# Kernel optimization log

Measured on AMD Instinct MI355X. Metric: run time of the kernel, lower is better.

The kernel has to match this reference:

```python
import jax, jax.numpy as jnp
import numpy as np

IMAGE_W = 640
IMAGE_H = 640
MIN_SCORE = 0.05
NMS_THR = 0.5
MAX_DET = 100
B, A, C = 8, 76725, 80  # batch, total anchors over FPN levels (640x640, 9 anchors/loc), COCO classes


def setup_inputs() -> dict:
    key = jax.random.key(0)
    k1, k2, k3, k4, k5, k6 = jax.random.split(key, 6)
    # sigmoid-like class scores in [0,1]
    cls_heads = jax.random.uniform(k1, (B, A, C), dtype=jnp.float32)
    reg_heads = jax.random.normal(k2, (B, A, 4), dtype=jnp.float32) * 0.5
    # plausible anchors: centers in image, sizes in [16,256]
    cx = jax.random.uniform(k3, (B, A), dtype=jnp.float32) * IMAGE_W
    cy = jax.random.uniform(k4, (B, A), dtype=jnp.float32) * IMAGE_H
    w = jax.random.uniform(k5, (B, A), dtype=jnp.float32, minval=16.0, maxval=256.0)
    h = jax.random.uniform(k6, (B, A), dtype=jnp.float32, minval=16.0, maxval=256.0)
    batch_anchors = jnp.stack([cx - 0.5 * w, cy - 0.5 * h, cx + 0.5 * w, cy + 0.5 * h], axis=-1)
    return {"cls_heads": cls_heads, "reg_heads": reg_heads, "batch_anchors": batch_anchors}


def _decode(reg, anchors):
    # snap_tx_ty_tw_th_to_x1_y1_x2_y2: [A,4] deltas + [A,4] anchors -> int boxes
    wh = anchors[:, 2:] - anchors[:, :2]
    ctr = anchors[:, :2] + 0.5 * wh
    reg = reg * jnp.array([0.1, 0.1, 0.2, 0.2], dtype=reg.dtype)
    pwh = jnp.exp(reg[:, 2:]) * wh
    pctr = reg[:, :2] * wh + ctr
    boxes = jnp.concatenate([pctr - 0.5 * pwh, pctr + 0.5 * pwh], axis=1)
    boxes = boxes.astype(jnp.int32)  # torch .int() truncates toward zero, same as astype
    x1 = jnp.maximum(boxes[:, 0], 0)
    y1 = jnp.maximum(boxes[:, 1], 0)
    x2 = jnp.minimum(boxes[:, 2], IMAGE_W - 1)
    y2 = jnp.minimum(boxes[:, 3], IMAGE_H - 1)
    return jnp.stack([x1, y1, x2, y2], axis=1)


def _single_image(cls, reg, anchors):
    boxes = _decode(reg, anchors)              # [A,4] int32
    bf = boxes.astype(jnp.float32)
    scores = jnp.max(cls, axis=1)              # [A]
    classes = jnp.argmax(cls, axis=1)          # [A] int
    areas = (bf[:, 2] - bf[:, 0]) * (bf[:, 3] - bf[:, 1])
    work = jnp.where(scores > MIN_SCORE, scores, -jnp.inf)
    out_s = jnp.full((MAX_DET,), -1.0, jnp.float32)
    out_c = jnp.full((MAX_DET,), -1.0, jnp.float32)
    out_b = jnp.full((MAX_DET, 4), -1.0, jnp.float32)

    # Greedy global pick + per-class suppression == per-class NMS followed by
    # global descending sort + top MAX_DET (classes are independent under NMS).
    def body(i, carry):
        work, out_s, out_c, out_b = carry
        idx = jnp.argmax(work)
        s = work[idx]
        ok = jnp.isfinite(s)
        box = bf[idx]
        cls_i = classes[idx]
        xx1 = jnp.maximum(bf[:, 0], box[0])
        yy1 = jnp.maximum(bf[:, 1], box[1])
        xx2 = jnp.minimum(bf[:, 2], box[2])
        yy2 = jnp.minimum(bf[:, 3], box[3])
        inter = jnp.maximum(xx2 - xx1, 0.0) * jnp.maximum(yy2 - yy1, 0.0)
        union = areas + areas[idx] - inter
        iou = jnp.where(union > 0, inter / jnp.where(union > 0, union, 1.0), 0.0)
        suppress = (classes == cls_i) & (iou >= NMS_THR)  # keep mask was iou < thr
        work = jnp.where(ok & suppress, -jnp.inf, work)
        work = work.at[idx].set(-jnp.inf)
        out_s = out_s.at[i].set(jnp.where(ok, s, -1.0))
        out_c = out_c.at[i].set(jnp.where(ok, cls_i.astype(jnp.float32), -1.0))
        out_b = out_b.at[i].set(jnp.where(ok, box, -1.0))
        return (work, out_s, out_c, out_b)

    _, out_s, out_c, out_b = jax.lax.fori_loop(0, MAX_DET, body, (work, out_s, out_c, out_b))
    return out_s, out_c, out_b


def reference(cls_heads, reg_heads, batch_anchors):
    return jax.vmap(_single_image)(cls_heads, reg_heads, batch_anchors)
```

## Files before the change

### kernel.cpp

```cpp
#include <hip/hip_runtime.h>

#define NB 8
#define NA 76725
#define NC 80
#define MAXDET 100
#define CAP  1024
#define FTHR 0x3F7FF994u
#define TILE 64
#define NBLK 1199
#define ST4  21

__device__ inline unsigned long long shfl_down_u64(unsigned long long v, int o) {
    unsigned lo = (unsigned)v, hi = (unsigned)(v >> 32);
    lo = __shfl_down(lo, o);
    hi = __shfl_down(hi, o);
    return ((unsigned long long)hi << 32) | lo;
}

__device__ inline unsigned long long shfl_xor_u64(unsigned long long v, int m) {
    unsigned lo = __shfl_xor((unsigned)v, m), hi = __shfl_xor((unsigned)(v >> 32), m);
    return ((unsigned long long)hi << 32) | lo;
}

__device__ inline bool iou_ge_half(float ax1, float ay1, float ax2, float ay2, float aar,
                                   float bx1, float by1, float bx2, float by2, float bar) {
    float xx1 = fmaxf(ax1, bx1), yy1 = fmaxf(ay1, by1);
    float xx2 = fminf(ax2, bx2), yy2 = fminf(ay2, by2);
    float inter = fmaxf(xx2 - xx1, 0.0f) * fmaxf(yy2 - yy1, 0.0f);
    float un = aar + bar - inter;
    float iou = (un > 0.0f) ? inter / un : 0.0f;
    return iou >= 0.5f;
}

__global__ __launch_bounds__(256) void k_map(const float* __restrict__ cls,
                                             const float* __restrict__ reg,
                                             const float* __restrict__ anc,
                                             unsigned long long* __restrict__ keys,
                                             unsigned long long* __restrict__ boxes,
                                             ulonglong2* __restrict__ cand,
                                             unsigned int* __restrict__ cnt_p,
                                             unsigned int* __restrict__ vws) {
    __shared__ float4 sc[TILE * ST4];
    __shared__ unsigned s_v[4];
    const int b = blockIdx.y;
    const int n0 = blockIdx.x * TILE;
    const int ait = min(TILE, NA - n0);
    const int tid = threadIdx.x;
    const size_t base4 = ((size_t)b * NA + n0) * (NC / 4);
    const int nq = ait * (NC / 4);

#pragma unroll
    for (int k = 0; k < 5; ++k) {
        int q = tid + k * 256;
        if (q < nq) {
            float4 v = reinterpret_cast<const float4*>(cls)[base4 + q];
            sc[(q / 20) * ST4 + (q % 20)] = v;
        }
    }
    __syncthreads();

    const int a = tid >> 2, t = tid & 3;
    float best = -1.0f; int bc = 0;
#pragma unroll
    for (int j = 0; j < 5; ++j) {
        float4 v = sc[a * ST4 + t * 5 + j];
        if (v.x > best) { best = v.x; bc = t * 20 + 4 * j + 0; }
        if (v.y > best) { best = v.y; bc = t * 20 + 4 * j + 1; }
        if (v.z > best) { best = v.z; bc = t * 20 + 4 * j + 2; }
        if (v.w > best) { best = v.w; bc = t * 20 + 4 * j + 3; }
    }
    unsigned long long pk = ((unsigned long long)__float_as_uint(best) << 8)
                          | (unsigned)(255 - bc);
    pk = max(pk, shfl_xor_u64(pk, 1));
    pk = max(pk, shfl_xor_u64(pk, 2));

    bool valid = false, sel = false;
    unsigned long long key = 0ull, bp = 0ull;
    if (t == 0 && a < ait) {
        unsigned sbits = (unsigned)(pk >> 8);
        int cg = 255 - (int)(pk & 0xFFull);
        const int n_img = n0 + a;
        const size_t n = (size_t)b * NA + n_img;
        float4 rg = reinterpret_cast<const float4*>(reg)[n];
        float4 an = reinterpret_cast<const float4*>(anc)[n];

        float wx = __fsub_rn(an.z, an.x);
        float wy = __fsub_rn(an.w, an.y);
        float cx = __fadd_rn(an.x, __fmul_rn(0.5f, wx));
        float cy = __fadd_rn(an.y, __fmul_rn(0.5f, wy));
        float tx = __fmul_rn(rg.x, 0.1f), ty = __fmul_rn(rg.y, 0.1f);
        float tw = __fmul_rn(rg.z, 0.2f), th = __fmul_rn(rg.w, 0.2f);
        float pw = __fmul_rn(expf(tw), wx);
        float ph = __fmul_rn(expf(th), wy);
        float px = __fadd_rn(__fmul_rn(tx, wx), cx);
        float py = __fadd_rn(__fmul_rn(ty, wy), cy);
        int x1 = (int)__fsub_rn(px, __fmul_rn(0.5f, pw));
        int y1 = (int)__fsub_rn(py, __fmul_rn(0.5f, ph));
        int x2 = (int)__fadd_rn(px, __fmul_rn(0.5f, pw));
        int y2 = (int)__fadd_rn(py, __fmul_rn(0.5f, ph));
        x1 = max(x1, 0); y1 = max(y1, 0); x2 = min(x2, 639); y2 = min(y2, 639);

        bp = (unsigned long long)(unsigned short)(short)x1
           | ((unsigned long long)(unsigned short)(short)y1 << 16)
           | ((unsigned long long)(unsigned short)(short)x2 << 32)
           | ((unsigned long long)(unsigned short)(short)y2 << 48);
        float bestf = __uint_as_float(sbits);
        if (bestf > 0.05f) {
            unsigned inv = 0x1FFFFu - (unsigned)n_img;
            key = ((unsigned long long)sbits << 32) | ((unsigned long long)inv << 7)
                | (unsigned)cg;
            valid = true;
            sel = sbits >= FTHR;
        }
        keys[n] = key;
        boxes[n] = bp;
    }

    const int lane = tid & 63;
    const int wid = tid >> 6;

    unsigned long long bal = __ballot(valid);
    if (lane == 0) s_v[wid] = (unsigned)__popcll(bal);

    unsigned long long sbal = __ballot(sel);
    unsigned base = 0;
    if (lane == 0 && sbal) base = atomicAdd(&cnt_p[b * 32], (unsigned)__popcll(sbal));
    base = __shfl(base, 0);
    if (sel) {
        unsigned off = base + (unsigned)__popcll(sbal & ((1ull << lane) - 1ull));
        if (off < CAP) {
            ulonglong2 e; e.x = key; e.y = bp;
            cand[(size_t)b * CAP + off] = e;
        }
    }

    __syncthreads();
    if (tid == 0)
        vws[(size_t)b * NBLK + blockIdx.x] = s_v[0] + s_v[1] + s_v[2] + s_v[3];
}

__global__ __launch_bounds__(512) void k_nms(const ulonglong2* __restrict__ cand,
                                             const unsigned int* __restrict__ cnt_p,
                                             const unsigned int* __restrict__ vws,
                                             unsigned int* __restrict__ flag,
                                             float* __restrict__ out) {
    __shared__ unsigned long long sk[CAP];
    __shared__ unsigned long long sb[CAP];
    __shared__ int s_np;
    __shared__ unsigned s_ws[8];
    __shared__ unsigned s_vsum;
    const int b = blockIdx.x;
    unsigned total = cnt_p[b * 32];
    bool overflow = total > CAP;
    unsigned m = overflow ? CAP : total;

    unsigned local = 0;
    for (int j = threadIdx.x; j < NBLK; j += 512) local += vws[(size_t)b * NBLK + j];
    for (int o = 32; o > 0; o >>= 1) local += __shfl_down(local, o);
    if ((threadIdx.x & 63) == 0) s_ws[threadIdx.x >> 6] = local;

    for (int i = threadIdx.x; i < CAP; i += 512) {
        if (i < (int)m) { ulonglong2 e = cand[(size_t)b * CAP + i]; sk[i] = e.x; sb[i] = e.y; }
        else            { sk[i] = 0ull; sb[i] = 0ull; }
    }
    __syncthreads();
    if (threadIdx.x == 0) {
        unsigned s = 0;
        for (int w = 0; w < 8; ++w) s += s_ws[w];
        s_vsum = s;
    }

    for (int k = 2; k <= CAP; k <<= 1) {
        for (int j = k >> 1; j > 0; j >>= 1) {
            __syncthreads();
            int t = threadIdx.x;
            int i = ((t & ~(j - 1)) << 1) | (t & (j - 1));
            int l = i | j;
            unsigned long long ki = sk[i], kl = sk[l];
            bool desc = (i & k) == 0;
            if (desc ? (ki < kl) : (ki > kl)) {
                sk[i] = kl; sk[l] = ki;
                unsigned long long tmp = sb[i]; sb[i] = sb[l]; sb[l] = tmp;
            }
        }
    }
    __syncthreads();

    if (threadIdx.x < 64) {
        const int lane = threadIdx.x;
        float q0x1 = 0, q0y1 = 0, q0x2 = 0, q0y2 = 0, q0a = 0; int q0c = -1;
        float q1x1 = 0, q1y1 = 0, q1x2 = 0, q1y2 = 0, q1a = 0; int q1c = -1;
        int np = 0;
        unsigned long long nk = (m > 0) ? sk[0] : 0ull;
        unsigned long long nbx = (m > 0) ? sb[0] : 0ull;
        for (int jj = 0; jj < (int)m && np < MAXDET; ++jj) {
            unsigned long long key = nk;
            unsigned long long bx = nbx;
            if (jj + 1 < (int)m) { nk = sk[jj + 1]; nbx = sb[jj + 1]; }
            if (!key) break;
            int ci = (int)(key & 0x7Full);
            float x1 = (float)(short)(bx & 0xFFFF);
            float y1 = (float)(short)((bx >> 16) & 0xFFFF);
            float x2 = (float)(short)((bx >> 32) & 0xFFFF);
            float y2 = (float)(short)((bx >> 48) & 0xFFFF);
            float ar = (x2 - x1) * (y2 - y1);
            bool sup = false;
            if (lane < np && q0c == ci)
                sup = iou_ge_half(q0x1, q0y1, q0x2, q0y2, q0a, x1, y1, x2, y2, ar);
            if (64 + lane < np && q1c == ci)
                sup = sup || iou_ge_half(q1x1, q1y1, q1x2, q1y2, q1a, x1, y1, x2, y2, ar);
            if (__ballot(sup) != 0ull) continue;
            int s = np;
            if (s < 64) {
                if (lane == s) {
                    q0x1 = x1; q0y1 = y1; q0x2 = x2; q0y2 = y2; q0a = ar; q0c = ci;
                    out[b * MAXDET + s] = __uint_as_float((unsigned)(key >> 32));
                    out[NB * MAXDET + b * MAXDET + s] = (float)ci;
                    float* ob = out + 2 * NB * MAXDET + (size_t)(b * MAXDET + s) * 4;
                    ob[0] = x1; ob[1] = y1; ob[2] = x2; ob[3] = y2;
                }
            } else {
                if (lane == s - 64) {
                    q1x1 = x1; q1y1 = y1; q1x2 = x2; q1y2 = y2; q1a = ar; q1c = ci;
                    out[b * MAXDET + s] = __uint_as_float((unsigned)(key >> 32));
                    out[NB * MAXDET + b * MAXDET + s] = (float)ci;
                    float* ob = out + 2 * NB * MAXDET + (size_t)(b * MAXDET + s) * 4;
                    ob[0] = x1; ob[1] = y1; ob[2] = x2; ob[3] = y2;
                }
            }
            ++np;
        }
        if (lane == 0) s_np = np;
    }
    __syncthreads();
    int np = s_np;
    bool fb = overflow || (np < MAXDET && s_vsum > m);
    if (threadIdx.x == 0) flag[b] = fb ? 1u : 0u;
    if (!fb) {
        for (int i = np + (int)threadIdx.x; i < MAXDET; i += 512) {
            out[b * MAXDET + i] = -1.0f;
            out[NB * MAXDET + b * MAXDET + i] = -1.0f;
            float* ob = out + 2 * NB * MAXDET + (size_t)(b * MAXDET + i) * 4;
            ob[0] = -1.0f; ob[1] = -1.0f; ob[2] = -1.0f; ob[3] = -1.0f;
        }
    }
}

__global__ __launch_bounds__(1024) void k_fallback(unsigned long long* __restrict__ keys,
                                                   const unsigned long long* __restrict__ boxes,
                                                   const unsigned int* __restrict__ flag,
                                                   float* __restrict__ out) {
    const int b = blockIdx.x;
    if (!flag[b]) return;
    __shared__ unsigned long long wm[16];
    __shared__ unsigned long long gbest;
    unsigned long long* kb = keys + (size_t)b * NA;
    const unsigned long long* bb = boxes + (size_t)b * NA;

    for (int it = 0; it < MAXDET; ++it) {
        unsigned long long best = 0ull;
        for (int i = threadIdx.x; i < NA; i += 1024) {
            unsigned long long k = kb[i];
            if (k > best) best = k;
        }
        for (int o = 32; o > 0; o >>= 1) {
            unsigned long long v = shfl_down_u64(best, o);
            if (v > best) best = v;
        }
        if ((threadIdx.x & 63) == 0) wm[threadIdx.x >> 6] = best;
        __syncthreads();
        if (threadIdx.x == 0) {
            unsigned long long g = wm[0];
            for (int w = 1; w < 16; ++w) if (wm[w] > g) g = wm[w];
            gbest = g;
        }
        __syncthreads();
        best = gbest;
        if (best == 0ull) {
            for (int s = it + (int)threadIdx.x; s < MAXDET; s += 1024) {
                out[b * MAXDET + s] = -1.0f;
                out[NB * MAXDET + b * MAXDET + s] = -1.0f;
                float* ob = out + 2 * NB * MAXDET + (size_t)(b * MAXDET + s) * 4;
                ob[0] = -1.0f; ob[1] = -1.0f; ob[2] = -1.0f; ob[3] = -1.0f;
            }
            break;
        }
        int ci = (int)(best & 0x7Full);
        int a = 0x1FFFF - (int)((best >> 7) & 0x1FFFFull);
        unsigned long long bx = bb[a];
        float x1 = (float)(short)(bx & 0xFFFF);
        float y1 = (float)(short)((bx >> 16) & 0xFFFF);
        float x2 = (float)(short)((bx >> 32) & 0xFFFF);
        float y2 = (float)(short)((bx >> 48) & 0xFFFF);
        float ar = (x2 - x1) * (y2 - y1);
        if (threadIdx.x == 0) {
            out[b * MAXDET + it] = __uint_as_float((unsigned)(best >> 32));
            out[NB * MAXDET + b * MAXDET + it] = (float)ci;
            float* ob = out + 2 * NB * MAXDET + (size_t)(b * MAXDET + it) * 4;
            ob[0] = x1; ob[1] = y1; ob[2] = x2; ob[3] = y2;
        }
        for (int i = threadIdx.x; i < NA; i += 1024) {
            unsigned long long kk = kb[i];
            if (!kk) continue;
            if (kk == best) { kb[i] = 0ull; continue; }
            if ((int)(kk & 0x7Full) != ci) continue;
            unsigned long long ob2 = bb[i];
            float u1 = (float)(short)(ob2 & 0xFFFF);
            float v1 = (float)(short)((ob2 >> 16) & 0xFFFF);
            float u2 = (float)(short)((ob2 >> 32) & 0xFFFF);
            float v2 = (float)(short)((ob2 >> 48) & 0xFFFF);
            float oar = (u2 - u1) * (v2 - v1);
            if (iou_ge_half(x1, y1, x2, y2, ar, u1, v1, u2, v2, oar)) kb[i] = 0ull;
        }
        __syncthreads();
    }
}

extern "C" void kernel_launch(void* const* d_in, const int* in_sizes, int n_in,
                              void* d_out, int out_size, void* d_ws, size_t ws_size,
                              hipStream_t stream) {
    const float* cls = (const float*)d_in[0];
    const float* reg = (const float*)d_in[1];
    const float* anc = (const float*)d_in[2];
    float* out = (float*)d_out;

    const size_t SZ_KEYS = (size_t)NB * NA * 8;
    unsigned long long* keys  = (unsigned long long*)d_ws;
    unsigned long long* boxes = (unsigned long long*)((char*)d_ws + SZ_KEYS);
    ulonglong2* cand = (ulonglong2*)((char*)d_ws + 2 * SZ_KEYS);
    unsigned* cnt_p = (unsigned*)((char*)d_ws + 2 * SZ_KEYS + (size_t)NB * CAP * 16);
    unsigned* vws   = cnt_p + NB * 32;
    unsigned* flag  = vws + (size_t)NB * NBLK;

    hipMemsetAsync(cnt_p, 0, NB * 32 * 4, stream);

    dim3 gmap(NBLK, NB);
    k_map<<<gmap, 256, 0, stream>>>(cls, reg, anc, keys, boxes, cand, cnt_p, vws);
    k_nms<<<NB, 512, 0, stream>>>(cand, cnt_p, vws, flag, out);
    k_fallback<<<NB, 1024, 0, stream>>>(keys, boxes, flag, out);
}
```

Before: 333.8 us.

## Make k_map persistent with register-prefetched next tile loads

Replaces the one-block-per-tile grid with a persistent grid of 192 blocks per image. Each block loops over tiles and prefetches the next tile's class scores, regression and anchor data into registers while it computes the current tile. Reg and anchor data are staged through shared memory, and the per-block valid counts shrink to 192 entries per image, which k_nms reads. This aims to hide global load latency in a memory-bound pass, at the cost of more registers per thread and lower occupancy.

Measured after the change: 333.0 us. Within noise of the previous version (-0.2%).

```diff
diff --git a/kernel.cpp b/kernel.cpp
--- a/kernel.cpp
+++ b/kernel.cpp
@@ -8,6 +8,7 @@
 #define FTHR 0x3F7FF994u
 #define TILE 64
 #define NBLK 1199
+#define GX   192
 #define ST4  21
 
 __device__ inline unsigned long long shfl_down_u64(unsigned long long v, int o) {
@@ -41,102 +42,131 @@
                                              unsigned int* __restrict__ cnt_p,
                                              unsigned int* __restrict__ vws) {
     __shared__ float4 sc[TILE * ST4];
+    __shared__ float4 s_rg[TILE];
+    __shared__ float4 s_an[TILE];
     __shared__ unsigned s_v[4];
     const int b = blockIdx.y;
-    const int n0 = blockIdx.x * TILE;
-    const int ait = min(TILE, NA - n0);
     const int tid = threadIdx.x;
-    const size_t base4 = ((size_t)b * NA + n0) * (NC / 4);
-    const int nq = ait * (NC / 4);
-
-#pragma unroll
-    for (int k = 0; k < 5; ++k) {
-        int q = tid + k * 256;
-        if (q < nq) {
-            float4 v = reinterpret_cast<const float4*>(cls)[base4 + q];
-            sc[(q / 20) * ST4 + (q % 20)] = v;
-        }
-    }
-    __syncthreads();
-
-    const int a = tid >> 2, t = tid & 3;
-    float best = -1.0f; int bc = 0;
-#pragma unroll
-    for (int j = 0; j < 5; ++j) {
-        float4 v = sc[a * ST4 + t * 5 + j];
-        if (v.x > best) { best = v.x; bc = t * 20 + 4 * j + 0; }
-        if (v.y > best) { best = v.y; bc = t * 20 + 4 * j + 1; }
-        if (v.z > best) { best = v.z; bc = t * 20 + 4 * j + 2; }
-        if (v.w > best) { best = v.w; bc = t * 20 + 4 * j + 3; }
-    }
-    unsigned long long pk = ((unsigned long long)__float_as_uint(best) << 8)
-                          | (unsigned)(255 - bc);
-    pk = max(pk, shfl_xor_u64(pk, 1));
-    pk = max(pk, shfl_xor_u64(pk, 2));
-
-    bool valid = false, sel = false;
-    unsigned long long key = 0ull, bp = 0ull;
-    if (t == 0 && a < ait) {
-        unsigned sbits = (unsigned)(pk >> 8);
-        int cg = 255 - (int)(pk & 0xFFull);
-        const int n_img = n0 + a;
-        const size_t n = (size_t)b * NA + n_img;
-        float4 rg = reinterpret_cast<const float4*>(reg)[n];
-        float4 an = reinterpret_cast<const float4*>(anc)[n];
-
-        float wx = __fsub_rn(an.z, an.x);
-        float wy = __fsub_rn(an.w, an.y);
-        float cx = __fadd_rn(an.x, __fmul_rn(0.5f, wx));
-        float cy = __fadd_rn(an.y, __fmul_rn(0.5f, wy));
-        float tx = __fmul_rn(rg.x, 0.1f), ty = __fmul_rn(rg.y, 0.1f);
-        float tw = __fmul_rn(rg.z, 0.2f), th = __fmul_rn(rg.w, 0.2f);
-        float pw = __fmul_rn(expf(tw), wx);
-        float ph = __fmul_rn(expf(th), wy);
-        float px = __fadd_rn(__fmul_rn(tx, wx), cx);
-        float py = __fadd_rn(__fmul_rn(ty, wy), cy);
-        int x1 = (int)__fsub_rn(px, __fmul_rn(0.5f, pw));
-        int y1 = (int)__fsub_rn(py, __fmul_rn(0.5f, ph));
-        int x2 = (int)__fadd_rn(px, __fmul_rn(0.5f, pw));
-        int y2 = (int)__fadd_rn(py, __fmul_rn(0.5f, ph));
-        x1 = max(x1, 0); y1 = max(y1, 0); x2 = min(x2, 639); y2 = min(y2, 639);
-
-        bp = (unsigned long long)(unsigned short)(short)x1
-           | ((unsigned long long)(unsigned short)(short)y1 << 16)
-           | ((unsigned long long)(unsigned short)(short)x2 << 32)
-           | ((unsigned long long)(unsigned short)(short)y2 << 48);
-        float bestf = __uint_as_float(sbits);
-        if (bestf > 0.05f) {
-            unsigned inv = 0x1FFFFu - (unsigned)n_img;
-            key = ((unsigned long long)sbits << 32) | ((unsigned long long)inv << 7)
-                | (unsigned)cg;
-            valid = true;
-            sel = sbits >= FTHR;
-        }
-        keys[n] = key;
-        boxes[n] = bp;
-    }
-
     const int lane = tid & 63;
     const int wid = tid >> 6;
-
-    unsigned long long bal = __ballot(valid);
-    if (lane == 0) s_v[wid] = (unsigned)__popcll(bal);
-
-    unsigned long long sbal = __ballot(sel);
-    unsigned base = 0;
-    if (lane == 0 && sbal) base = atomicAdd(&cnt_p[b * 32], (unsigned)__popcll(sbal));
-    base = __shfl(base, 0);
-    if (sel) {
-        unsigned off = base + (unsigned)__popcll(sbal & ((1ull << lane) - 1ull));
-        if (off < CAP) {
-            ulonglong2 e; e.x = key; e.y = bp;
-            cand[(size_t)b * CAP + off] = e;
-        }
-    }
-
+    const float4* cls4 = reinterpret_cast<const float4*>(cls);
+    const float4* reg4 = reinterpret_cast<const float4*>(reg);
+    const float4* anc4 = reinterpret_cast<const float4*>(anc);
+
+    int tile = blockIdx.x;
+    int n0 = tile * TILE;
+    int ait = min(TILE, NA - n0);
+    int nq = ait * 20;
+    size_t base4 = ((size_t)b * NA + n0) * 20;
+
+    float4 r0, r1, r2, r3, r4, ra;
+#define LOADQ(K, RK) { int q = tid + (K)*256; if (q < nq) RK = cls4[base4 + q]; }
+    LOADQ(0, r0) LOADQ(1, r1) LOADQ(2, r2) LOADQ(3, r3) LOADQ(4, r4)
+    if (tid < 64) { if (tid < ait) ra = reg4[(size_t)b * NA + n0 + tid]; }
+    else if (tid < 128) { if (tid - 64 < ait) ra = anc4[(size_t)b * NA + n0 + tid - 64]; }
+
+    unsigned vacc = 0;
+    for (;;) {
+        __syncthreads();
+#define STQ(K, RK) { int q = tid + (K)*256; if (q < nq) sc[(q / 20) * ST4 + (q % 20)] = RK; }
+        STQ(0, r0) STQ(1, r1) STQ(2, r2) STQ(3, r3) STQ(4, r4)
+        if (tid < 64) { if (tid < ait) s_rg[tid] = ra; }
+        else if (tid < 128) { if (tid - 64 < ait) s_an[tid - 64] = ra; }
+        __syncthreads();
+
+        const int cn0 = n0, cait = ait;
+
+        tile += GX;
+        const bool more = tile < NBLK;
+        if (more) {
+            n0 = tile * TILE;
+            ait = min(TILE, NA - n0);
+            nq = ait * 20;
+            base4 = ((size_t)b * NA + n0) * 20;
+            LOADQ(0, r0) LOADQ(1, r1) LOADQ(2, r2) LOADQ(3, r3) LOADQ(4, r4)
+            if (tid < 64) { if (tid < ait) ra = reg4[(size_t)b * NA + n0 + tid]; }
+            else if (tid < 128) { if (tid - 64 < ait) ra = anc4[(size_t)b * NA + n0 + tid - 64]; }
+        }
+
+        const int a = tid >> 2, t = tid & 3;
+        float best = -1.0f; int bc = 0;
+#pragma unroll
+        for (int j = 0; j < 5; ++j) {
+            float4 v = sc[a * ST4 + t * 5 + j];
+            if (v.x > best) { best = v.x; bc = t * 20 + 4 * j + 0; }
+            if (v.y > best) { best = v.y; bc = t * 20 + 4 * j + 1; }
+            if (v.z > best) { best = v.z; bc = t * 20 + 4 * j + 2; }
+            if (v.w > best) { best = v.w; bc = t * 20 + 4 * j + 3; }
+        }
+        unsigned long long pk = ((unsigned long long)__float_as_uint(best) << 8)
+                              | (unsigned)(255 - bc);
+        pk = max(pk, shfl_xor_u64(pk, 1));
+        pk = max(pk, shfl_xor_u64(pk, 2));
+
+        bool valid = false, sel = false;
+        unsigned long long key = 0ull, bp = 0ull;
+        if (t == 0 && a < cait) {
+            unsigned sbits = (unsigned)(pk >> 8);
+            int cg = 255 - (int)(pk & 0xFFull);
+            const int n_img = cn0 + a;
+            const size_t n = (size_t)b * NA + n_img;
+            float4 rg = s_rg[a];
+            float4 an = s_an[a];
+
+            float wx = __fsub_rn(an.z, an.x);
+            float wy = __fsub_rn(an.w, an.y);
+            float cx = __fadd_rn(an.x, __fmul_rn(0.5f, wx));
+            float cy = __fadd_rn(an.y, __fmul_rn(0.5f, wy));
+            float tx = __fmul_rn(rg.x, 0.1f), ty = __fmul_rn(rg.y, 0.1f);
+            float tw = __fmul_rn(rg.z, 0.2f), th = __fmul_rn(rg.w, 0.2f);
+            float pw = __fmul_rn(expf(tw), wx);
+            float ph = __fmul_rn(expf(th), wy);
+            float px = __fadd_rn(__fmul_rn(tx, wx), cx);
+            float py = __fadd_rn(__fmul_rn(ty, wy), cy);
+            int x1 = (int)__fsub_rn(px, __fmul_rn(0.5f, pw));
+            int y1 = (int)__fsub_rn(py, __fmul_rn(0.5f, ph));
+            int x2 = (int)__fadd_rn(px, __fmul_rn(0.5f, pw));
+            int y2 = (int)__fadd_rn(py, __fmul_rn(0.5f, ph));
+            x1 = max(x1, 0); y1 = max(y1, 0); x2 = min(x2, 639); y2 = min(y2, 639);
+
+            bp = (unsigned long long)(unsigned short)(short)x1
+               | ((unsigned long long)(unsigned short)(short)y1 << 16)
+               | ((unsigned long long)(unsigned short)(short)x2 << 32)
+               | ((unsigned long long)(unsigned short)(short)y2 << 48);
+            float bestf = __uint_as_float(sbits);
+            if (bestf > 0.05f) {
+                unsigned inv = 0x1FFFFu - (unsigned)n_img;
+                key = ((unsigned long long)sbits << 32) | ((unsigned long long)inv << 7)
+                    | (unsigned)cg;
+                valid = true;
+                sel = sbits >= FTHR;
+            }
+            keys[n] = key;
+            boxes[n] = bp;
+        }
+
+        unsigned long long bal = __ballot(valid);
+        if (lane == 0) vacc += (unsigned)__popcll(bal);
+
+        unsigned long long sbal = __ballot(sel);
+        unsigned base = 0;
+        if (lane == 0 && sbal) base = atomicAdd(&cnt_p[b * 32], (unsigned)__popcll(sbal));
+        base = __shfl(base, 0);
+        if (sel) {
+            unsigned off = base + (unsigned)__popcll(sbal & ((1ull << lane) - 1ull));
+            if (off < CAP) {
+                ulonglong2 e; e.x = key; e.y = bp;
+                cand[(size_t)b * CAP + off] = e;
+            }
+        }
+
+        if (!more) break;
+    }
+
+    if (lane == 0) s_v[wid] = vacc;
     __syncthreads();
     if (tid == 0)
-        vws[(size_t)b * NBLK + blockIdx.x] = s_v[0] + s_v[1] + s_v[2] + s_v[3];
+        vws[(size_t)b * GX + blockIdx.x] = s_v[0] + s_v[1] + s_v[2] + s_v[3];
 }
 
 __global__ __launch_bounds__(512) void k_nms(const ulonglong2* __restrict__ cand,
@@ -155,7 +185,7 @@
     unsigned m = overflow ? CAP : total;
 
     unsigned local = 0;
-    for (int j = threadIdx.x; j < NBLK; j += 512) local += vws[(size_t)b * NBLK + j];
+    for (int j = threadIdx.x; j < GX; j += 512) local += vws[(size_t)b * GX + j];
     for (int o = 32; o > 0; o >>= 1) local += __shfl_down(local, o);
     if ((threadIdx.x & 63) == 0) s_ws[threadIdx.x >> 6] = local;
 
@@ -330,11 +360,11 @@
     ulonglong2* cand = (ulonglong2*)((char*)d_ws + 2 * SZ_KEYS);
     unsigned* cnt_p = (unsigned*)((char*)d_ws + 2 * SZ_KEYS + (size_t)NB * CAP * 16);
     unsigned* vws   = cnt_p + NB * 32;
-    unsigned* flag  = vws + (size_t)NB * NBLK;
+    unsigned* flag  = vws + (size_t)NB * GX;
 
     hipMemsetAsync(cnt_p, 0, NB * 32 * 4, stream);
 
-    dim3 gmap(NBLK, NB);
+    dim3 gmap(GX, NB);
     k_map<<<gmap, 256, 0, stream>>>(cls, reg, anc, keys, boxes, cand, cnt_p, vws);
     k_nms<<<NB, 512, 0, stream>>>(cand, cnt_p, vws, flag, out);
     k_fallback<<<NB, 1024, 0, stream>>>(keys, boxes, flag, out);
```
